# Kernel tuning notes

Hardware: AMD Instinct MI355X
Metric: run time of the kernel (lower is better)

The kernel has to match this reference:

```python
import math
import jax, jax.numpy as jnp
import numpy as np

HEADS = 8
DIM_HEAD = 32
DIM = 128
EPS_LN = 1e-5
EPS_NORM = 1e-12


def setup_inputs() -> dict:
    key = jax.random.key(0)
    ks = jax.random.split(key, 4)
    inner = HEADS * DIM_HEAD  # 256
    x = jax.random.normal(ks[0], (1, DIM, 16, 64, 64), dtype=jnp.float32)
    g = jnp.ones((1, DIM, 1, 1, 1), dtype=jnp.float32)
    b = jnp.zeros((1, DIM, 1, 1, 1), dtype=jnp.float32)
    w_qkv = jax.random.normal(ks[1], (3 * inner, DIM), dtype=jnp.float32) * 0.05
    w_out = jax.random.normal(ks[2], (DIM, inner), dtype=jnp.float32) * 0.05
    b_out = jnp.zeros((DIM,), dtype=jnp.float32)
    return {"x": x, "g": g, "b": b, "w_qkv": w_qkv, "w_out": w_out, "b_out": b_out}


def _l2norm_ch(t):
    # F.normalize(t, dim=1): divide by max(||t||_2, eps) along channel axis
    n = jnp.sqrt(jnp.sum(t * t, axis=1, keepdims=True))
    return t / jnp.maximum(n, EPS_NORM)


def _gather_axis(t, idx, axis):
    # t: [bh, c, D, H, W]; idx: [bh, kk]; gather along spatial `axis`
    shape = list(t.shape)
    shape[axis] = idx.shape[1]
    ix = idx.reshape((idx.shape[0],) + (1,) * (axis - 1) + (idx.shape[1],) + (1,) * (4 - axis))
    ix = jnp.broadcast_to(ix, shape)
    return jnp.take_along_axis(t, ix, axis=axis)


def _dpsa_forward(x, g, b, w_qkv, w_out, b_out):
    bsz, c, D, H, W = x.shape
    kd = int(math.ceil(D ** 0.5))
    kh = int(math.ceil(H ** 0.5))
    kw = int(math.ceil(W ** 0.5))

    # ChanLayerNorm3d (biased variance over channel dim)
    mean = jnp.mean(x, axis=1, keepdims=True)
    var = jnp.var(x, axis=1, keepdims=True)
    xn = (x - mean) / jnp.sqrt(var + EPS_LN) * g + b

    # 1x1x1 conv to qkv (no bias)
    qkv = jnp.einsum('oc,bcdhw->bodhw', w_qkv, xn)
    inner = HEADS * DIM_HEAD
    q, k, v = qkv[:, :inner], qkv[:, inner:2 * inner], qkv[:, 2 * inner:]

    def fold(t):  # b (i c) d h w -> (b i) c d h w
        return t.reshape(bsz * HEADS, DIM_HEAD, D, H, W)
    q, k, v = fold(q), fold(k), fold(v)
    D0, H0, W0 = D, H, W

    q = _l2norm_ch(q)
    k = _l2norm_ch(k)
    q_abs = jnp.abs(q)

    # depth pruning
    if kd < D:
        q_probe = q_abs.sum(axis=(3, 4))                 # [bh, c, D]
        k_probe = jnp.abs(k).sum(axis=(3, 4))            # [bh, c, D]
        score = jnp.einsum('bcd,bcd->bd', q_probe, k_probe)
        _, idx = jax.lax.top_k(score, kd)
        k = _gather_axis(k, idx, 2)
        v = _gather_axis(v, idx, 2)
        D = kd
    # height pruning
    if kh < H:
        q_probe = q_abs.sum(axis=(2, 4))                 # [bh, c, H]
        k_probe = jnp.abs(k).sum(axis=(2, 4))            # [bh, c, H]
        score = jnp.einsum('bch,bch->bh', q_probe, k_probe)
        _, idx = jax.lax.top_k(score, kh)
        k = _gather_axis(k, idx, 3)
        v = _gather_axis(v, idx, 3)
        H = kh
    # width pruning
    if kw < W:
        q_probe = q_abs.sum(axis=(2, 3))                 # [bh, c, W]
        k_probe = jnp.abs(k).sum(axis=(2, 3))            # [bh, c, W]
        score = jnp.einsum('bcw,bcw->bw', q_probe, k_probe)
        _, idx = jax.lax.top_k(score, kw)
        k = _gather_axis(k, idx, 4)
        v = _gather_axis(v, idx, 4)
        W = kw

    def flat(t):  # b c d h w -> b (dhw) c
        return t.reshape(t.shape[0], t.shape[1], -1).transpose(0, 2, 1)
    qf, kf, vf = flat(q), flat(k), flat(v)

    sim = jnp.einsum('bic,bjc->bij', qf, kf)  # note: original applies no scale
    attn = jax.nn.softmax(sim, axis=-1)
    out_flat = jnp.einsum('bij,bjc->bic', attn, vf)  # [bh, N, c]

    # faithful to torch .view: raw row-major reinterpretation
    out = out_flat.reshape(bsz * HEADS, DIM_HEAD, D0, H0, W0)
    out = out.reshape(bsz, HEADS * DIM_HEAD, D0, H0, W0)
    return jnp.einsum('oc,bcdhw->bodhw', w_out, out) + b_out[None, :, None, None, None]


def reference(x, g, b, w_qkv, w_out, b_out):
    return _dpsa_forward(x, g, b, w_qkv, w_out, b_out)
```

## Files before the change

### kernel.cpp

```cpp
#include <hip/hip_runtime.h>
#include <math.h>

#define P_TOT 65536
#define CH    128
#define NHEAD 8
#define KD    4
#define KH    8
#define KW    8
#define NJ    256

typedef unsigned short u16;
typedef unsigned int   u32;
typedef __attribute__((ext_vector_type(8))) short frag8;
typedef __attribute__((ext_vector_type(4))) float f32x4;

__device__ inline u16 bf16r(float a) {
    u32 ua = __float_as_uint(a);
    return (u16)((ua + 0x7fff + ((ua >> 16) & 1)) >> 16);
}
__device__ inline float bf16f(u16 h) {
    return __uint_as_float(((u32)h) << 16);
}
__device__ inline u32 packhl(float v) {
    u16 hh = bf16r(v);
    u16 ll = bf16r(v - bf16f(hh));
    return (u32)hh | ((u32)ll << 16);
}

__global__ __launch_bounds__(256) void k_ln(const float* __restrict__ x,
                                            const float* __restrict__ g,
                                            const float* __restrict__ b,
                                            u16* __restrict__ xn_hi,
                                            u16* __restrict__ xn_lo) {
    __shared__ u32 buf[64 * 131];
    __shared__ float red[8 * 64];
    __shared__ float stat[2 * 64];
    float* xt = (float*)buf;
    int t  = threadIdx.x;
    int p0 = blockIdx.x * 64;
    #pragma unroll
    for (int r = 0; r < 8; ++r) {
        int id = t + 256 * r;
        int c = id >> 4, q4 = id & 15;
        *(float4*)(xt + c * 64 + q4 * 4) =
            *(const float4*)(x + (size_t)c * P_TOT + p0 + q4 * 4);
    }
    __syncthreads();
    int pp = t & 63, part = t >> 6;
    float sum = 0.f, ssq = 0.f;
    for (int ci = 0; ci < 32; ++ci) {
        float v = xt[(part * 32 + ci) * 64 + pp];
        sum += v; ssq += v * v;
    }
    red[part * 64 + pp] = sum;
    red[256 + part * 64 + pp] = ssq;
    __syncthreads();
    if (t < 64) {
        float s = red[t] + red[64 + t] + red[128 + t] + red[192 + t];
        float q = red[256 + t] + red[320 + t] + red[384 + t] + red[448 + t];
        float mean = s * (1.f / CH);
        float var  = q * (1.f / CH) - mean * mean;
        stat[t] = mean;
        stat[64 + t] = 1.f / sqrtf(var + 1e-5f);
    }
    __syncthreads();
    float mean = stat[pp], inv = stat[64 + pp];
    u32 pk[32];
    for (int ci = 0; ci < 32; ++ci) {
        int c = part * 32 + ci;
        float v  = xt[c * 64 + pp];
        float xn = (v - mean) * inv * g[c] + b[c];
        pk[ci] = packhl(xn);
    }
    __syncthreads();
    u32* tr = buf;
    for (int ci = 0; ci < 32; ++ci)
        tr[pp * 131 + part * 32 + ci] = pk[ci];
    __syncthreads();
    #pragma unroll
    for (int r = 0; r < 8; ++r) {
        int id = t + 256 * r;
        int pr = id >> 5, ch = id & 31;
        const u32* srcp = tr + pr * 131 + ch * 4;
        u32 v0 = srcp[0], v1 = srcp[1], v2 = srcp[2], v3 = srcp[3];
        uint2 hv, lv;
        hv.x = __builtin_amdgcn_perm(v1, v0, 0x05040100);
        hv.y = __builtin_amdgcn_perm(v3, v2, 0x05040100);
        lv.x = __builtin_amdgcn_perm(v1, v0, 0x07060302);
        lv.y = __builtin_amdgcn_perm(v3, v2, 0x07060302);
        size_t off = (size_t)(p0 + pr) * 128 + ch * 4;
        *(uint2*)(xn_hi + off) = hv;
        *(uint2*)(xn_lo + off) = lv;
    }
}

__global__ __launch_bounds__(256) void k_wsplit(const float* __restrict__ wqkv,
                                                const float* __restrict__ wout,
                                                u16* __restrict__ w_hi,
                                                u16* __restrict__ w_lo,
                                                u16* __restrict__ w2_hi,
                                                u16* __restrict__ w2_lo) {
    int id = blockIdx.x * 256 + threadIdx.x;
    if (id < 65536) {
        float v = wqkv[id];
        u16 hh = bf16r(v);
        w_hi[id] = hh; w_lo[id] = bf16r(v - bf16f(hh));
    } else {
        int j = id - 65536;
        float v = wout[j];
        u16 hh = bf16r(v);
        w2_hi[j] = hh; w2_lo[j] = bf16r(v - bf16f(hh));
    }
}

__global__ __launch_bounds__(256) void k_gemm_qkv(const u16* __restrict__ xn_hi,
                                                  const u16* __restrict__ xn_lo,
                                                  const u16* __restrict__ w_hi,
                                                  const u16* __restrict__ w_lo,
                                                  float* __restrict__ qk,
                                                  u16* __restrict__ qT) {
    __shared__ u16 smem[4 * 128 * 64];
    u16* a_hi = smem;
    u16* a_lo = smem + 8192;
    u16* b_hi = smem + 16384;
    u16* b_lo = smem + 24576;
    int t    = threadIdx.x;
    int lane = t & 63, wave = t >> 6;
    int wp = wave & 1, wo = wave >> 1;
    int m = lane & 15, quad = lane >> 4;
    int p0 = blockIdx.x * 128;
    int o0 = blockIdx.y * 128;
    f32x4 acc[4][4] = {};
    for (int k0 = 0; k0 < 128; k0 += 64) {
        __syncthreads();
        #pragma unroll
        for (int r = 0; r < 4; ++r) {
            int id  = t + 256 * r;
            int row = id >> 3, gg = id & 7;
            int gs  = gg ^ (row & 7);
            int dst = row * 64 + gg * 8;
            size_t sa = (size_t)(p0 + row) * 128 + k0 + gs * 8;
            size_t sb = (size_t)(o0 + row) * 128 + k0 + gs * 8;
            *(uint4*)(a_hi + dst) = *(const uint4*)(xn_hi + sa);
            *(uint4*)(a_lo + dst) = *(const uint4*)(xn_lo + sa);
            *(uint4*)(b_hi + dst) = *(const uint4*)(w_hi + sb);
            *(uint4*)(b_lo + dst) = *(const uint4*)(w_lo + sb);
        }
        __syncthreads();
        #pragma unroll
        for (int ks = 0; ks < 2; ++ks) {
            frag8 ah[4], al[4], bh[4], bl[4];
            #pragma unroll
            for (int i = 0; i < 4; ++i) {
                int row = wp * 64 + i * 16 + m;
                int gg  = (ks * 4 + quad) ^ (row & 7);
                ah[i] = *(const frag8*)(a_hi + row * 64 + gg * 8);
                al[i] = *(const frag8*)(a_lo + row * 64 + gg * 8);
            }
            #pragma unroll
            for (int j = 0; j < 4; ++j) {
                int row = wo * 64 + j * 16 + m;
                int gg  = (ks * 4 + quad) ^ (row & 7);
                bh[j] = *(const frag8*)(b_hi + row * 64 + gg * 8);
                bl[j] = *(const frag8*)(b_lo + row * 64 + gg * 8);
            }
            #pragma unroll
            for (int i = 0; i < 4; ++i)
                #pragma unroll
                for (int j = 0; j < 4; ++j) {
                    acc[i][j] = __builtin_amdgcn_mfma_f32_16x16x32_bf16(ah[i], bh[j], acc[i][j], 0, 0, 0);
                    acc[i][j] = __builtin_amdgcn_mfma_f32_16x16x32_bf16(ah[i], bl[j], acc[i][j], 0, 0, 0);
                    acc[i][j] = __builtin_amdgcn_mfma_f32_16x16x32_bf16(al[i], bh[j], acc[i][j], 0, 0, 0);
                }
        }
    }
    #pragma unroll
    for (int i = 0; i < 4; ++i) {
        #pragma unroll
        for (int jg = 0; jg < 2; ++jg) {
            f32x4 s;
            #pragma unroll
            for (int r = 0; r < 4; ++r)
                s[r] = acc[i][2 * jg][r] * acc[i][2 * jg][r]
                     + acc[i][2 * jg + 1][r] * acc[i][2 * jg + 1][r];
            #pragma unroll
            for (int mask = 1; mask <= 8; mask <<= 1) {
                s[0] += __shfl_xor(s[0], mask, 64);
                s[1] += __shfl_xor(s[1], mask, 64);
                s[2] += __shfl_xor(s[2], mask, 64);
                s[3] += __shfl_xor(s[3], mask, 64);
            }
            #pragma unroll
            for (int r = 0; r < 4; ++r) {
                float inv = 1.f / fmaxf(sqrtf(s[r]), 1e-12f);
                acc[i][2 * jg][r]     *= inv;
                acc[i][2 * jg + 1][r] *= inv;
            }
        }
    }
    #pragma unroll
    for (int i = 0; i < 4; ++i) {
        int p = p0 + wp * 64 + i * 16 + quad * 4;
        #pragma unroll
        for (int j = 0; j < 4; ++j) {
            int o = o0 + wo * 64 + j * 16 + m;
            float4 v;
            v.x = acc[i][j][0]; v.y = acc[i][j][1];
            v.z = acc[i][j][2]; v.w = acc[i][j][3];
            *(float4*)(qk + (size_t)o * P_TOT + p) = v;
        }
    }
    if (o0 < 256) {
        __syncthreads();
        u16* qtb = smem;
        #pragma unroll
        for (int i = 0; i < 4; ++i)
            #pragma unroll
            for (int j = 0; j < 4; ++j) {
                int grp = wo * 2 + (j >> 1);
                int c   = (j & 1) * 16 + m;
                #pragma unroll
                for (int r = 0; r < 4; ++r) {
                    int pl = wp * 64 + i * 16 + quad * 4 + r;
                    qtb[grp * 5120 + pl * 40 + c] = bf16r(acc[i][j][r]);
                }
            }
        __syncthreads();
        int gbase = o0 >> 5;
        #pragma unroll
        for (int ri = 0; ri < 8; ++ri) {
            int id = t + 256 * ri;
            int grp = id >> 9, rem = id & 511;
            int pl = rem >> 2, cq = rem & 3;
            uint4 v = *(const uint4*)(qtb + grp * 5120 + pl * 40 + cq * 8);
            *(uint4*)(qT + ((size_t)(gbase + grp) * P_TOT + p0 + pl) * 32 + cq * 8) = v;
        }
    }
}

__global__ __launch_bounds__(256) void k_probe(const float* __restrict__ qk,
                                               float* __restrict__ pd,
                                               float* __restrict__ pdh,
                                               float* __restrict__ pdw) {
    int o = blockIdx.x;
    int d = blockIdx.y;
    int t = threadIdx.x;
    __shared__ float ph2[64 * 65];
    __shared__ float pwl[256];
    for (int i = t; i < 64 * 65; i += 256) ph2[i] = 0.f;
    __syncthreads();
    const float* src = qk + o * P_TOT + d * 4096;
    int col = t & 63;
    int tg  = t >> 6;
    float wsum = 0.f;
    #pragma unroll
    for (int r = 0; r < 16; ++r) {
        int i = t + 256 * r;
        float val = fabsf(src[i]);
        wsum += val;
        int h = 4 * r + tg;
        ph2[h * 65 + col] += val;
    }
    pwl[t] = wsum;
    __syncthreads();
    if (t < 64) {
        float s = 0.f;
        for (int cc = 0; cc < 64; ++cc) s += ph2[t * 65 + cc];
        pdh[(o * 16 + d) * 64 + t] = s;
        ph2[t * 65 + 64] = s;
    } else if (t < 128) {
        int w = t - 64;
        float s = 0.f;
        for (int g2 = 0; g2 < 4; ++g2) s += pwl[g2 * 64 + w];
        pdw[(o * 16 + d) * 64 + w] = s;
    }
    __syncthreads();
    if (t == 0) {
        float s = 0.f;
        for (int h = 0; h < 64; ++h) s += ph2[h * 65 + 64];
        pd[o * 16 + d] = s;
    }
}

__global__ __launch_bounds__(64) void k_psum(const float* __restrict__ pdh,
                                             const float* __restrict__ pdw,
                                             float* __restrict__ qph,
                                             float* __restrict__ qpw) {
    int o = blockIdx.x, t = threadIdx.x;
    float sh = 0.f, sw = 0.f;
    #pragma unroll
    for (int d = 0; d < 16; ++d) {
        sh += pdh[(o * 16 + d) * 64 + t];
        sw += pdw[(o * 16 + d) * 64 + t];
    }
    qph[o * 64 + t] = sh;
    qpw[o * 64 + t] = sw;
}

__global__ __launch_bounds__(64) void k_topk_d(const float* __restrict__ pd,
                                               int* __restrict__ idx_d) {
    int h = blockIdx.x, t = threadIdx.x;
    __shared__ float sc[16];
    if (t < 16) {
        float s = 0.f;
        for (int c = 0; c < 32; ++c)
            s += pd[(h * 32 + c) * 16 + t] * pd[(256 + h * 32 + c) * 16 + t];
        sc[t] = s;
    }
    __syncthreads();
    if (t == 0) {
        bool used[16] = {};
        for (int r = 0; r < KD; ++r) {
            int best = 0; float bv = -1e30f;
            for (int i = 0; i < 16; ++i)
                if (!used[i] && sc[i] > bv) { bv = sc[i]; best = i; }
            used[best] = true;
            idx_d[h * KD + r] = best;
        }
    }
}

__global__ __launch_bounds__(256) void k_topk_h(const float* __restrict__ qph,
                                                const float* __restrict__ pdh,
                                                const int* __restrict__ idx_d,
                                                int* __restrict__ idx_h) {
    int h = blockIdx.x, t = threadIdx.x;
    int tq = t & 63, cg = t >> 6;
    __shared__ float sc2[4][64];
    __shared__ float sc[64];
    int ds[KD];
    #pragma unroll
    for (int i = 0; i < KD; ++i) ds[i] = idx_d[h * KD + i];
    float partial = 0.f;
    for (int ci = 0; ci < 8; ++ci) {
        int c  = cg * 8 + ci;
        int oq = h * 32 + c, ok = 256 + h * 32 + c;
        float qp = qph[oq * 64 + tq];
        float kp = 0.f;
        #pragma unroll
        for (int i = 0; i < KD; ++i) kp += pdh[(ok * 16 + ds[i]) * 64 + tq];
        partial += qp * kp;
    }
    sc2[cg][tq] = partial;
    __syncthreads();
    if (t < 64) sc[t] = sc2[0][t] + sc2[1][t] + sc2[2][t] + sc2[3][t];
    __syncthreads();
    if (t == 0) {
        bool used[64] = {};
        for (int r = 0; r < KH; ++r) {
            int best = 0; float bv = -1e30f;
            for (int i = 0; i < 64; ++i)
                if (!used[i] && sc[i] > bv) { bv = sc[i]; best = i; }
            used[best] = true;
            idx_h[h * KH + r] = best;
        }
    }
}

__global__ __launch_bounds__(64) void k_probe_w(const float* __restrict__ qk,
                                                const int* __restrict__ idx_d,
                                                const int* __restrict__ idx_h,
                                                float* __restrict__ kpw) {
    int o2 = blockIdx.x;
    int w  = threadIdx.x;
    int h  = o2 >> 5;
    const float* src = qk + (256 + o2) * P_TOT;
    float s = 0.f;
    for (int i = 0; i < KD; ++i) {
        int pb = idx_d[h * KD + i] * 4096;
        for (int j = 0; j < KH; ++j)
            s += fabsf(src[pb + idx_h[h * KH + j] * 64 + w]);
    }
    kpw[o2 * 64 + w] = s;
}

__global__ __launch_bounds__(256) void k_topk_w(const float* __restrict__ qpw,
                                                const float* __restrict__ kpw,
                                                int* __restrict__ idx_w) {
    int h = blockIdx.x, t = threadIdx.x;
    int tq = t & 63, cg = t >> 6;
    __shared__ float sc2[4][64];
    __shared__ float sc[64];
    float partial = 0.f;
    for (int ci = 0; ci < 8; ++ci) {
        int c  = cg * 8 + ci;
        int oq = h * 32 + c;
        partial += qpw[oq * 64 + tq] * kpw[(h * 32 + c) * 64 + tq];
    }
    sc2[cg][tq] = partial;
    __syncthreads();
    if (t < 64) sc[t] = sc2[0][t] + sc2[1][t] + sc2[2][t] + sc2[3][t];
    __syncthreads();
    if (t == 0) {
        bool used[64] = {};
        for (int r = 0; r < KW; ++r) {
            int best = 0; float bv = -1e30f;
            for (int i = 0; i < 64; ++i)
                if (!used[i] && sc[i] > bv) { bv = sc[i]; best = i; }
            used[best] = true;
            idx_w[h * KW + r] = best;
        }
    }
}

__global__ __launch_bounds__(64) void k_gather(const float* __restrict__ qk,
                                               const u16* __restrict__ xn_hi,
                                               const u16* __restrict__ xn_lo,
                                               const float* __restrict__ wqkv,
                                               const int* __restrict__ idx_d,
                                               const int* __restrict__ idx_h,
                                               const int* __restrict__ idx_w,
                                               u16* __restrict__ kb,
                                               u16* __restrict__ vT) {
    int h  = blockIdx.x;
    int jb = blockIdx.y;
    int t  = threadIdx.x;
    int j  = jb * 2 + (t >> 5);
    int c  = t & 31;
    int di = j >> 6, hi = (j >> 3) & 7, wi = j & 7;
    int p  = idx_d[h * KD + di] * 4096 + idx_h[h * KH + hi] * 64 + idx_w[h * KW + wi];
    kb[(h * NJ + j) * 32 + c] = bf16r(qk[(256 + h * 32 + c) * P_TOT + p]);
    const float* wr = wqkv + (512 + h * 32 + c) * CH;
    const u16* xh = xn_hi + (size_t)p * 128;
    const u16* xl = xn_lo + (size_t)p * 128;
    float acc = 0.f;
    for (int cc = 0; cc < CH; ++cc) {
        float v = bf16f(xh[cc]) + bf16f(xl[cc]);
        acc += wr[cc] * v;
    }
    int pos = (j & 0xE0) | ((j & 0x0C) << 1) | ((j & 0x10) >> 2) | (j & 3);
    vT[((size_t)h * 32 + c) * NJ + pos] = bf16r(acc);
}

__device__ inline frag8 mk_frag(uint2 a, uint2 b) {
    union { u32 u[4]; frag8 f; } v;
    v.u[0] = a.x; v.u[1] = a.y; v.u[2] = b.x; v.u[3] = b.y;
    return v.f;
}

__global__ __launch_bounds__(256) void k_attn(const u16* __restrict__ qT,
                                              const u16* __restrict__ kb,
                                              const u16* __restrict__ vT,
                                              u32* __restrict__ attn_pk) {
    __shared__ u16 sK[256 * 32];
    __shared__ u16 sV[32 * 264];
    int h    = blockIdx.x >> 8;
    int pc   = blockIdx.x & 255;
    int wave = threadIdx.x >> 6;
    int lane = threadIdx.x & 63;
    int m    = lane & 15;
    int quad = lane >> 4;
    int t    = threadIdx.x;

    int qbase = pc * 256 + wave * 64;
    frag8 bq[4];
    #pragma unroll
    for (int i = 0; i < 4; ++i)
        bq[i] = *(const frag8*)(qT + ((size_t)h * P_TOT + qbase + i * 16 + m) * 32 + quad * 8);

    const uint4* kg  = (const uint4*)(kb + (size_t)h * NJ * 32);
    uint4*       sKg = (uint4*)sK;
    #pragma unroll
    for (int r = 0; r < 4; ++r)
        sKg[t + 256 * r] = kg[t + 256 * r];
    const uint4* vg = (const uint4*)(vT + (size_t)h * 32 * NJ);
    #pragma unroll
    for (int r = 0; r < 4; ++r) {
        int g2 = t + 256 * r;
        int row = g2 >> 5, col = g2 & 31;
        *(uint4*)(sV + row * 264 + col * 8) = vg[g2];
    }
    __syncthreads();

    f32x4 zero = {0.f, 0.f, 0.f, 0.f};
    #pragma unroll
    for (int tile = 0; tile < 4; ++tile) {
        int p = qbase + tile * 16 + m;
        float den = 0.f;
        uint2 pk[16];
        #pragma unroll
        for (int tt = 0; tt < 16; ++tt) {
            frag8 ak = *(const frag8*)(sK + (tt * 16 + m) * 32 + quad * 8);
            f32x4 st = __builtin_amdgcn_mfma_f32_16x16x32_bf16(ak, bq[tile], zero, 0, 0, 0);
            float e0 = __expf(st[0]);
            float e1 = __expf(st[1]);
            float e2 = __expf(st[2]);
            float e3 = __expf(st[3]);
            den += (e0 + e1) + (e2 + e3);
            pk[tt].x = __builtin_amdgcn_perm(__float_as_uint(e1), __float_as_uint(e0), 0x07060302);
            pk[tt].y = __builtin_amdgcn_perm(__float_as_uint(e3), __float_as_uint(e2), 0x07060302);
        }
        den += __shfl_xor(den, 16, 64);
        den += __shfl_xor(den, 32, 64);

        f32x4 a0e = zero, a0o = zero, a1e = zero, a1o = zero;
        #pragma unroll
        for (int jc = 0; jc < 8; jc += 2) {
            frag8 bp0  = mk_frag(pk[2 * jc],     pk[2 * jc + 1]);
            frag8 bp1  = mk_frag(pk[2 * jc + 2], pk[2 * jc + 3]);
            frag8 av00 = *(const frag8*)(sV + m * 264 + jc * 32 + quad * 8);
            frag8 av01 = *(const frag8*)(sV + m * 264 + (jc + 1) * 32 + quad * 8);
            frag8 av10 = *(const frag8*)(sV + (16 + m) * 264 + jc * 32 + quad * 8);
            frag8 av11 = *(const frag8*)(sV + (16 + m) * 264 + (jc + 1) * 32 + quad * 8);
            a0e = __builtin_amdgcn_mfma_f32_16x16x32_bf16(av00, bp0, a0e, 0, 0, 0);
            a0o = __builtin_amdgcn_mfma_f32_16x16x32_bf16(av01, bp1, a0o, 0, 0, 0);
            a1e = __builtin_amdgcn_mfma_f32_16x16x32_bf16(av10, bp0, a1e, 0, 0, 0);
            a1o = __builtin_amdgcn_mfma_f32_16x16x32_bf16(av11, bp1, a1o, 0, 0, 0);
        }
        f32x4 acc0 = a0e + a0o;
        f32x4 acc1 = a1e + a1o;
        float inv = 1.f / den;
        size_t base = ((size_t)(h * 32 + (p >> 11))) * P_TOT + (size_t)(p & 2047) * 32;
        uint4 o0, o1;
        o0.x = packhl(acc0[0] * inv); o0.y = packhl(acc0[1] * inv);
        o0.z = packhl(acc0[2] * inv); o0.w = packhl(acc0[3] * inv);
        o1.x = packhl(acc1[0] * inv); o1.y = packhl(acc1[1] * inv);
        o1.z = packhl(acc1[2] * inv); o1.w = packhl(acc1[3] * inv);
        *(uint4*)(attn_pk + base + quad * 4)      = o0;
        *(uint4*)(attn_pk + base + 16 + quad * 4) = o1;
    }
}

__global__ __launch_bounds__(256) void k_gemm_out(const u32* __restrict__ attn_pk,
                                                  const u16* __restrict__ w2_hi,
                                                  const u16* __restrict__ w2_lo,
                                                  const float* __restrict__ bout,
                                                  float* __restrict__ out) {
    __shared__ u16 a_hi[128 * 64], a_lo[128 * 64];
    __shared__ u16 b_hi[128 * 64], b_lo[128 * 64];
    int t    = threadIdx.x;
    int lane = t & 63, wave = t >> 6;
    int wq = wave & 1, wo = wave >> 1;
    int m = lane & 15, quad = lane >> 4;
    int q0 = blockIdx.x * 128;
    f32x4 acc[4][4] = {};
    for (int k0 = 0; k0 < 256; k0 += 64) {
        __syncthreads();
        #pragma unroll
        for (int r = 0; r < 4; ++r) {
            int id = t + 256 * r;
            int qq = id & 127, gsel = id >> 7;
            u32 pkk[8];
            #pragma unroll
            for (int e = 0; e < 8; ++e)
                pkk[e] = attn_pk[(size_t)(k0 + gsel * 8 + e) * P_TOT + q0 + qq];
            u32 hi4[4], lo4[4];
            #pragma unroll
            for (int e = 0; e < 4; ++e) {
                hi4[e] = __builtin_amdgcn_perm(pkk[2*e+1], pkk[2*e], 0x05040100);
                lo4[e] = __builtin_amdgcn_perm(pkk[2*e+1], pkk[2*e], 0x07060302);
            }
            int go = (gsel ^ (qq & 7)) * 8;
            *(uint4*)(a_hi + qq * 64 + go) = *(uint4*)hi4;
            *(uint4*)(a_lo + qq * 64 + go) = *(uint4*)lo4;
        }
        #pragma unroll
        for (int r = 0; r < 4; ++r) {
            int id  = t + 256 * r;
            int row = id >> 3, gg = id & 7;
            int go  = (gg ^ (row & 7)) * 8;
            *(uint4*)(b_hi + row * 64 + go) =
                *(const uint4*)(w2_hi + (size_t)row * 256 + k0 + gg * 8);
            *(uint4*)(b_lo + row * 64 + go) =
                *(const uint4*)(w2_lo + (size_t)row * 256 + k0 + gg * 8);
        }
        __syncthreads();
        #pragma unroll
        for (int ks = 0; ks < 2; ++ks) {
            frag8 ah[4], al[4], bh[4], bl[4];
            #pragma unroll
            for (int i = 0; i < 4; ++i) {
                int row = wq * 64 + i * 16 + m;
                int gg  = (ks * 4 + quad) ^ (row & 7);
                ah[i] = *(const frag8*)(a_hi + row * 64 + gg * 8);
                al[i] = *(const frag8*)(a_lo + row * 64 + gg * 8);
            }
            #pragma unroll
            for (int j = 0; j < 4; ++j) {
                int row = wo * 64 + j * 16 + m;
                int gg  = (ks * 4 + quad) ^ (row & 7);
                bh[j] = *(const frag8*)(b_hi + row * 64 + gg * 8);
                bl[j] = *(const frag8*)(b_lo + row * 64 + gg * 8);
            }
            #pragma unroll
            for (int i = 0; i < 4; ++i)
                #pragma unroll
                for (int j = 0; j < 4; ++j) {
                    acc[i][j] = __builtin_amdgcn_mfma_f32_16x16x32_bf16(ah[i], bh[j], acc[i][j], 0, 0, 0);
                    acc[i][j] = __builtin_amdgcn_mfma_f32_16x16x32_bf16(ah[i], bl[j], acc[i][j], 0, 0, 0);
                    acc[i][j] = __builtin_amdgcn_mfma_f32_16x16x32_bf16(al[i], bh[j], acc[i][j], 0, 0, 0);
                }
        }
    }
    #pragma unroll
    for (int j = 0; j < 4; ++j) {
        int o = wo * 64 + j * 16 + m;
        float bv = bout[o];
        #pragma unroll
        for (int i = 0; i < 4; ++i) {
            int q = q0 + wq * 64 + i * 16 + quad * 4;
            float4 v;
            v.x = acc[i][j][0] + bv; v.y = acc[i][j][1] + bv;
            v.z = acc[i][j][2] + bv; v.w = acc[i][j][3] + bv;
            *(float4*)(out + (size_t)o * P_TOT + q) = v;
        }
    }
}

extern "C" void kernel_launch(void* const* d_in, const int* in_sizes, int n_in,
                              void* d_out, int out_size, void* d_ws, size_t ws_size,
                              hipStream_t stream) {
    const float* x    = (const float*)d_in[0];
    const float* g    = (const float*)d_in[1];
    const float* b    = (const float*)d_in[2];
    const float* wqkv = (const float*)d_in[3];
    const float* wout = (const float*)d_in[4];
    const float* bout = (const float*)d_in[5];
    float* out = (float*)d_out;
    float* ws  = (float*)d_ws;

    u16*   xn_hi = (u16*)ws;
    u16*   xn_lo = xn_hi + (size_t)128 * P_TOT;
    float* qk   = ws + 8388608;
    u32*   attn_pk = (u32*)(qk + 256 * P_TOT);
    float* aux  = ws + 41943040;
    float* pd    = aux;
    float* pdh   = pd + 8192;
    float* pdw   = pdh + 524288;
    float* kpw   = pdw + 524288;
    float* qph   = kpw + 16384;
    float* qpw   = qph + 32768;
    int*   idx_d = (int*)(qpw + 32768);
    int*   idx_h = idx_d + 32;
    int*   idx_w = idx_h + 64;
    u16*   kb    = (u16*)(idx_w + 64);
    u16*   vT    = kb + 8 * NJ * 32;
    u16*   qT    = vT + 8 * 32 * NJ;
    u16*   w_hi  = qT + (size_t)8 * P_TOT * 32;
    u16*   w_lo  = w_hi + 512 * 128;
    u16*   w2_hi = w_lo + 512 * 128;
    u16*   w2_lo = w2_hi + 128 * 256;

    k_ln<<<1024, 256, 0, stream>>>(x, g, b, xn_hi, xn_lo);
    k_wsplit<<<384, 256, 0, stream>>>(wqkv, wout, w_hi, w_lo, w2_hi, w2_lo);
    k_gemm_qkv<<<dim3(512, 4), 256, 0, stream>>>(xn_hi, xn_lo, w_hi, w_lo, qk, qT);
    k_probe<<<dim3(512, 16), 256, 0, stream>>>(qk, pd, pdh, pdw);
    k_psum<<<512, 64, 0, stream>>>(pdh, pdw, qph, qpw);
    k_topk_d<<<8, 64, 0, stream>>>(pd, idx_d);
    k_topk_h<<<8, 256, 0, stream>>>(qph, pdh, idx_d, idx_h);
    k_probe_w<<<256, 64, 0, stream>>>(qk, idx_d, idx_h, kpw);
    k_topk_w<<<8, 256, 0, stream>>>(qpw, kpw, idx_w);
    k_gather<<<dim3(8, 128), 64, 0, stream>>>(qk, xn_hi, xn_lo, wqkv,
                                              idx_d, idx_h, idx_w, kb, vT);
    k_attn<<<2048, 256, 0, stream>>>(qT, kb, vT, attn_pk);
    k_gemm_out<<<512, 256, 0, stream>>>(attn_pk, w2_hi, w2_lo, bout, out);
}
```

Measured before the change: 341.2 us.

## Fuse abs-sum probe reductions into QKV GEMM epilogue and skip Q fp32 store

Computes the depth, height and width abs-sum probes directly from the QKV GEMM accumulators, using shuffles, LDS and atomics, instead of rereading the full fp32 q/k tensor in separate probe and psum kernels. The fp32 store of q is dropped because only its bf16 transposed copy and the probe sums are needed. The zero-initialisation of the atomic target buffers is folded into the weight-split kernel. This removes two launches and a large read of q/k plus the q write, at the cost of many global atomics and a longer GEMM epilogue.

```diff
diff --git a/kernel.cpp b/kernel.cpp
--- a/kernel.cpp
+++ b/kernel.cpp
@@ -99,8 +99,10 @@
                                                 u16* __restrict__ w_hi,
                                                 u16* __restrict__ w_lo,
                                                 u16* __restrict__ w2_hi,
-                                                u16* __restrict__ w2_lo) {
+                                                u16* __restrict__ w2_lo,
+                                                float* __restrict__ zbuf) {
     int id = blockIdx.x * 256 + threadIdx.x;
+    if (id < 40960) zbuf[id] = 0.f;
     if (id < 65536) {
         float v = wqkv[id];
         u16 hh = bf16r(v);
@@ -118,7 +120,11 @@
                                                   const u16* __restrict__ w_hi,
                                                   const u16* __restrict__ w_lo,
                                                   float* __restrict__ qk,
-                                                  u16* __restrict__ qT) {
+                                                  u16* __restrict__ qT,
+                                                  float* __restrict__ pd,
+                                                  float* __restrict__ pdh,
+                                                  float* __restrict__ qph,
+                                                  float* __restrict__ qpw) {
     __shared__ u16 smem[4 * 128 * 64];
     u16* a_hi = smem;
     u16* a_lo = smem + 8192;
@@ -198,19 +204,85 @@
             }
         }
     }
-    #pragma unroll
-    for (int i = 0; i < 4; ++i) {
-        int p = p0 + wp * 64 + i * 16 + quad * 4;
+    int pb = blockIdx.x;
+    int d  = pb >> 5;
+    int hh = (2 * pb + wp) & 63;
+    bool isQ = (o0 < 256);
+    {
+        float sj[4];
         #pragma unroll
         for (int j = 0; j < 4; ++j) {
-            int o = o0 + wo * 64 + j * 16 + m;
-            float4 v;
-            v.x = acc[i][j][0]; v.y = acc[i][j][1];
-            v.z = acc[i][j][2]; v.w = acc[i][j][3];
-            *(float4*)(qk + (size_t)o * P_TOT + p) = v;
-        }
-    }
-    if (o0 < 256) {
+            float s = 0.f;
+            #pragma unroll
+            for (int i = 0; i < 4; ++i)
+                #pragma unroll
+                for (int r = 0; r < 4; ++r)
+                    s += fabsf(acc[i][j][r]);
+            sj[j] = s;
+        }
+        #pragma unroll
+        for (int j = 0; j < 4; ++j) {
+            sj[j] += __shfl_xor(sj[j], 16, 64);
+            sj[j] += __shfl_xor(sj[j], 32, 64);
+        }
+        if (quad == 0) {
+            #pragma unroll
+            for (int j = 0; j < 4; ++j) {
+                int o = o0 + wo * 64 + j * 16 + m;
+                atomicAdd(pd + o * 16 + d, sj[j]);
+                if (isQ) atomicAdd(qph + o * 64 + hh, sj[j]);
+                else     pdh[((size_t)o * 16 + d) * 64 + hh] = sj[j];
+            }
+        }
+    }
+    if (isQ) {
+        float* qw = (float*)smem;
+        __syncthreads();
+        if (wp == 0) {
+            #pragma unroll
+            for (int j = 0; j < 4; ++j) {
+                int ol = wo * 64 + j * 16 + m;
+                #pragma unroll
+                for (int i = 0; i < 4; ++i)
+                    #pragma unroll
+                    for (int r = 0; r < 4; ++r)
+                        qw[(i * 16 + quad * 4 + r) * 132 + ol] = fabsf(acc[i][j][r]);
+            }
+        }
+        __syncthreads();
+        if (wp == 1) {
+            #pragma unroll
+            for (int j = 0; j < 4; ++j) {
+                int ol = wo * 64 + j * 16 + m;
+                #pragma unroll
+                for (int i = 0; i < 4; ++i)
+                    #pragma unroll
+                    for (int r = 0; r < 4; ++r)
+                        qw[(i * 16 + quad * 4 + r) * 132 + ol] += fabsf(acc[i][j][r]);
+            }
+        }
+        __syncthreads();
+        #pragma unroll
+        for (int ri = 0; ri < 32; ++ri) {
+            int id = t + 256 * ri;
+            int ol = id >> 6, w = id & 63;
+            atomicAdd(qpw + (size_t)(o0 + ol) * 64 + w, qw[w * 132 + ol]);
+        }
+    } else {
+        #pragma unroll
+        for (int i = 0; i < 4; ++i) {
+            int p = p0 + wp * 64 + i * 16 + quad * 4;
+            #pragma unroll
+            for (int j = 0; j < 4; ++j) {
+                int o = o0 + wo * 64 + j * 16 + m;
+                float4 v;
+                v.x = acc[i][j][0]; v.y = acc[i][j][1];
+                v.z = acc[i][j][2]; v.w = acc[i][j][3];
+                *(float4*)(qk + (size_t)o * P_TOT + p) = v;
+            }
+        }
+    }
+    if (isQ) {
         __syncthreads();
         u16* qtb = smem;
         #pragma unroll
@@ -236,65 +308,6 @@
             *(uint4*)(qT + ((size_t)(gbase + grp) * P_TOT + p0 + pl) * 32 + cq * 8) = v;
         }
     }
-}
-
-__global__ __launch_bounds__(256) void k_probe(const float* __restrict__ qk,
-                                               float* __restrict__ pd,
-                                               float* __restrict__ pdh,
-                                               float* __restrict__ pdw) {
-    int o = blockIdx.x;
-    int d = blockIdx.y;
-    int t = threadIdx.x;
-    __shared__ float ph2[64 * 65];
-    __shared__ float pwl[256];
-    for (int i = t; i < 64 * 65; i += 256) ph2[i] = 0.f;
-    __syncthreads();
-    const float* src = qk + o * P_TOT + d * 4096;
-    int col = t & 63;
-    int tg  = t >> 6;
-    float wsum = 0.f;
-    #pragma unroll
-    for (int r = 0; r < 16; ++r) {
-        int i = t + 256 * r;
-        float val = fabsf(src[i]);
-        wsum += val;
-        int h = 4 * r + tg;
-        ph2[h * 65 + col] += val;
-    }
-    pwl[t] = wsum;
-    __syncthreads();
-    if (t < 64) {
-        float s = 0.f;
-        for (int cc = 0; cc < 64; ++cc) s += ph2[t * 65 + cc];
-        pdh[(o * 16 + d) * 64 + t] = s;
-        ph2[t * 65 + 64] = s;
-    } else if (t < 128) {
-        int w = t - 64;
-        float s = 0.f;
-        for (int g2 = 0; g2 < 4; ++g2) s += pwl[g2 * 64 + w];
-        pdw[(o * 16 + d) * 64 + w] = s;
-    }
-    __syncthreads();
-    if (t == 0) {
-        float s = 0.f;
-        for (int h = 0; h < 64; ++h) s += ph2[h * 65 + 64];
-        pd[o * 16 + d] = s;
-    }
-}
-
-__global__ __launch_bounds__(64) void k_psum(const float* __restrict__ pdh,
-                                             const float* __restrict__ pdw,
-                                             float* __restrict__ qph,
-                                             float* __restrict__ qpw) {
-    int o = blockIdx.x, t = threadIdx.x;
-    float sh = 0.f, sw = 0.f;
-    #pragma unroll
-    for (int d = 0; d < 16; ++d) {
-        sh += pdh[(o * 16 + d) * 64 + t];
-        sw += pdw[(o * 16 + d) * 64 + t];
-    }
-    qph[o * 64 + t] = sh;
-    qpw[o * 64 + t] = sw;
 }
 
 __global__ __launch_bounds__(64) void k_topk_d(const float* __restrict__ pd,
@@ -625,12 +638,11 @@
     u32*   attn_pk = (u32*)(qk + 256 * P_TOT);
     float* aux  = ws + 41943040;
     float* pd    = aux;
-    float* pdh   = pd + 8192;
-    float* pdw   = pdh + 524288;
-    float* kpw   = pdw + 524288;
-    float* qph   = kpw + 16384;
-    float* qpw   = qph + 32768;
-    int*   idx_d = (int*)(qpw + 32768);
+    float* qph   = pd + 8192;
+    float* qpw   = qph + 16384;
+    float* pdh   = qpw + 16384;
+    float* kpw   = pdh + 524288;
+    int*   idx_d = (int*)(kpw + 16384);
     int*   idx_h = idx_d + 32;
     int*   idx_w = idx_h + 64;
     u16*   kb    = (u16*)(idx_w + 64);
@@ -642,10 +654,9 @@
     u16*   w2_lo = w2_hi + 128 * 256;
 
     k_ln<<<1024, 256, 0, stream>>>(x, g, b, xn_hi, xn_lo);
-    k_wsplit<<<384, 256, 0, stream>>>(wqkv, wout, w_hi, w_lo, w2_hi, w2_lo);
-    k_gemm_qkv<<<dim3(512, 4), 256, 0, stream>>>(xn_hi, xn_lo, w_hi, w_lo, qk, qT);
-    k_probe<<<dim3(512, 16), 256, 0, stream>>>(qk, pd, pdh, pdw);
-    k_psum<<<512, 64, 0, stream>>>(pdh, pdw, qph, qpw);
+    k_wsplit<<<384, 256, 0, stream>>>(wqkv, wout, w_hi, w_lo, w2_hi, w2_lo, pd);
+    k_gemm_qkv<<<dim3(512, 4), 256, 0, stream>>>(xn_hi, xn_lo, w_hi, w_lo,
+                                                 qk, qT, pd, pdh, qph, qpw);
     k_topk_d<<<8, 64, 0, stream>>>(pd, idx_d);
     k_topk_h<<<8, 256, 0, stream>>>(qph, pdh, idx_d, idx_h);
     k_probe_w<<<256, 64, 0, stream>>>(qk, idx_d, idx_h, kpw);
```

New measurement: 408.0 us. 19.6% more time.
